# Performance work log

Hardware: AMD Instinct MI355X
Metric: run time of the kernel (lower is better)

## Reference

```python
import jax, jax.numpy as jnp
import numpy as np

HIDDEN_DIM = 2048
NUM_EXPERTS = 64
TOP_K = 8
NUM_TOKENS = 16384


def setup_inputs() -> dict:
    key = jax.random.key(0)
    k_x, k_w, k_b = jax.random.split(key, 3)
    X = jax.random.normal(k_x, (NUM_TOKENS, HIDDEN_DIM), dtype=jnp.float32)
    # nn.Linear(hidden_dim, num_experts): weight [out, in], bias [out]
    bound = 1.0 / np.sqrt(HIDDEN_DIM)
    W_gate = jax.random.uniform(k_w, (NUM_EXPERTS, HIDDEN_DIM), jnp.float32, -bound, bound)
    b_gate = jax.random.uniform(k_b, (NUM_EXPERTS,), jnp.float32, -bound, bound)
    return {"X": X, "W_gate": W_gate, "b_gate": b_gate}


def reference(X, W_gate, b_gate):
    # gate linear: [T, H] @ [H, E] + [E] -> [T, E]
    router_logits = jnp.einsum('th,eh->te', X, W_gate) + b_gate
    # softmax in float32 (matches dtype=torch.float)
    router_probs = jax.nn.softmax(router_logits.astype(jnp.float32), axis=-1)
    # top-k over experts: [T, K]
    router_weights, selected_experts_indices = jax.lax.top_k(router_probs, TOP_K)
    router_weights = router_weights / jnp.sum(router_weights, axis=-1, keepdims=True)
    router_weights = router_weights.astype(X.dtype)
    # one-hot [T, K, E] -> permute(2,1,0) -> [E, K, T]
    expert_mask = jax.nn.one_hot(selected_experts_indices, NUM_EXPERTS, dtype=jnp.int64 if jax.config.jax_enable_x64 else jnp.int32)
    expert_mask = jnp.transpose(expert_mask, (2, 1, 0))
    return (router_logits, router_weights, selected_experts_indices.astype(jnp.int32), expert_mask)
```

## Files before the change

kernel.cpp:

```cpp
#include <hip/hip_runtime.h>

#define NT 16384
#define NH 2048
#define NE 64
#define TOPK 8

#define TB 32
#define NSTEP 64
#define CSTEP 8
#define NCHUNK (NSTEP / CSTEP)

#define LOFF 0
#define WOFF (NT * NE)
#define IOFF (WOFF + NT * TOPK)
#define MOFF (IOFF + NT * TOPK)

typedef __attribute__((ext_vector_type(8))) short short8;
typedef __attribute__((ext_vector_type(4))) float floatx4;

union FragU { uint4 u; short8 s; };

#define WAITVM(n) asm volatile("s_waitcnt vmcnt(" #n ")" ::: "memory")
#define LGKM0     asm volatile("s_waitcnt lgkmcnt(0)" ::: "memory")

__device__ __forceinline__ void glds16(const void* g, void* l) {
    __builtin_amdgcn_global_load_lds(
        (const __attribute__((address_space(1))) unsigned int*)g,
        (__attribute__((address_space(3))) unsigned int*)l, 16, 0, 0);
}

__device__ __forceinline__ unsigned pack3(float a, float b, unsigned& w1, unsigned& w2) {
    unsigned au = __float_as_uint(a), bu = __float_as_uint(b);
    unsigned ah0 = au & 0xFFFF0000u, bh0 = bu & 0xFFFF0000u;
    float ra = a - __uint_as_float(ah0);
    float rb = b - __uint_as_float(bh0);
    unsigned ar = __float_as_uint(ra), br = __float_as_uint(rb);
    unsigned ah1 = ar & 0xFFFF0000u, bh1 = br & 0xFFFF0000u;
    float sa = ra - __uint_as_float(ah1);
    float sb = rb - __uint_as_float(bh1);
    w1 = bh1 | (ah1 >> 16);
    w2 = (__float_as_uint(sb) & 0xFFFF0000u) | (__float_as_uint(sa) >> 16);
    return bh0 | (ah0 >> 16);
}

__global__ __launch_bounds__(256)
void prep_kernel(const float* __restrict__ Wg, uint4* __restrict__ wsp,
                 float* __restrict__ out) {
    const int b = blockIdx.x;
    const int tid = threadIdx.x;

    float4 z = make_float4(0.f, 0.f, 0.f, 0.f);
    float4* mp = (float4*)(out + MOFF) + (size_t)b * 8192 + tid;
#pragma unroll
    for (int it = 0; it < 32; it++) mp[it * 256] = z;

    if (tid < 64) {
        const int t = b >> 2, g = b & 3;
        const int l = tid;
        const int e  = g * 16 + (l & 15);
        const int k0 = t * 32 + (l >> 4) * 8;
        const float* src = Wg + (size_t)e * NH + k0;
        float4 w0 = *(const float4*)src;
        float4 w1 = *(const float4*)(src + 4);
        unsigned u1[4], u2[4];
        uint4 p0;
        p0.x = pack3(w0.x, w0.y, u1[0], u2[0]);
        p0.y = pack3(w0.z, w0.w, u1[1], u2[1]);
        p0.z = pack3(w1.x, w1.y, u1[2], u2[2]);
        p0.w = pack3(w1.z, w1.w, u1[3], u2[3]);
        uint4* dst = wsp + (size_t)((t * 4 + g) * 3) * 64 + l;
        dst[0]   = p0;
        dst[64]  = make_uint4(u1[0], u1[1], u1[2], u1[3]);
        dst[128] = make_uint4(u2[0], u2[1], u2[2], u2[3]);
    }
}

__global__ __launch_bounds__(256, 2)
void router_kernel(const float* __restrict__ X, const uint4* __restrict__ wsp,
                   const float* __restrict__ bg, float* __restrict__ out) {
    __shared__ float SB[2][TB][256];
    __shared__ float Ls[TB][68];

    const int tid = threadIdx.x;
    const int wv  = tid >> 6;
    const int l   = tid & 63;
    const int th  = wv >> 1;
    const int eh  = wv & 1;
    const int lr  = l & 15, lq = l >> 4;
    const int lr7 = lr & 7;
    const int tbase = blockIdx.x * TB;

    floatx4 acc[2];
    acc[0] = (floatx4)0.0f;
    acc[1] = (floatx4)0.0f;

    const float* xsrc = X + (size_t)(tbase + wv * 8) * NH;
    const uint4* wb   = wsp + l;

#define STAGE(c_, s_) do { \
    _Pragma("unroll") \
    for (int j_ = 0; j_ < 8; j_++) \
        glds16(xsrc + (size_t)j_ * NH + (c_) * 256 + ((l ^ j_) << 2), \
               &SB[s_][wv * 8 + j_][0]); \
} while (0)

#define MFMA6(accv, A0, A1, A2, B0, B1, B2) do { \
    accv = __builtin_amdgcn_mfma_f32_16x16x32_bf16(A0, B0, accv, 0, 0, 0); \
    accv = __builtin_amdgcn_mfma_f32_16x16x32_bf16(A0, B1, accv, 0, 0, 0); \
    accv = __builtin_amdgcn_mfma_f32_16x16x32_bf16(A1, B0, accv, 0, 0, 0); \
    accv = __builtin_amdgcn_mfma_f32_16x16x32_bf16(A1, B1, accv, 0, 0, 0); \
    accv = __builtin_amdgcn_mfma_f32_16x16x32_bf16(A0, B2, accv, 0, 0, 0); \
    accv = __builtin_amdgcn_mfma_f32_16x16x32_bf16(A2, B0, accv, 0, 0, 0); \
} while (0)

#define KSTEP(s_, sg_, j_) do { \
    const float* ar_ = &SB[s_][th * 16 + lr][0]; \
    float4 lo_ = *(const float4*)(ar_ + ((((j_) * 8 + lq * 2 + 0) ^ lr7) << 2)); \
    float4 hi_ = *(const float4*)(ar_ + ((((j_) * 8 + lq * 2 + 1) ^ lr7) << 2)); \
    const uint4* wt_ = wb + ((size_t)(sg_) * 12 + eh * 6) * 64; \
    FragU b00, b01, b02, b10, b11, b12; \
    b00.u = wt_[0];   b01.u = wt_[64];  b02.u = wt_[128]; \
    b10.u = wt_[192]; b11.u = wt_[256]; b12.u = wt_[320]; \
    FragU a0_, a1_, a2_; \
    { unsigned u1_[4], u2_[4]; uint4 q_; \
      q_.x = pack3(lo_.x, lo_.y, u1_[0], u2_[0]); \
      q_.y = pack3(lo_.z, lo_.w, u1_[1], u2_[1]); \
      q_.z = pack3(hi_.x, hi_.y, u1_[2], u2_[2]); \
      q_.w = pack3(hi_.z, hi_.w, u1_[3], u2_[3]); \
      a0_.u = q_; \
      a1_.u = make_uint4(u1_[0], u1_[1], u1_[2], u1_[3]); \
      a2_.u = make_uint4(u2_[0], u2_[1], u2_[2], u2_[3]); } \
    __builtin_amdgcn_s_setprio(1); \
    MFMA6(acc[0], a0_.s, a1_.s, a2_.s, b00.s, b01.s, b02.s); \
    MFMA6(acc[1], a0_.s, a1_.s, a2_.s, b10.s, b11.s, b12.s); \
    __builtin_amdgcn_s_setprio(0); \
} while (0)

    STAGE(0, 0);
    STAGE(1, 1);

    WAITVM(8);
    __builtin_amdgcn_s_barrier();
#pragma unroll
    for (int j = 0; j < 8; j++) KSTEP(0, j, j);
    LGKM0;
    __builtin_amdgcn_s_barrier();
    STAGE(2, 0);

#pragma unroll 1
    for (int c = 1; c < NCHUNK; c++) {
        const int slot = c & 1;
        WAITVM(40);
        __builtin_amdgcn_s_barrier();
#pragma unroll
        for (int j = 0; j < 8; j++) KSTEP(slot, c * 8 + j, j);
        LGKM0;
        __builtin_amdgcn_s_barrier();
        if (c < NCHUNK - 2) STAGE(c + 2, slot);
    }

    const float b0 = bg[eh * 32 + lr];
    const float b1 = bg[eh * 32 + 16 + lr];
#pragma unroll
    for (int rr = 0; rr < 4; rr++) {
        Ls[th * 16 + lq * 4 + rr][eh * 32 + lr]      = acc[0][rr] + b0;
        Ls[th * 16 + lq * 4 + rr][eh * 32 + 16 + lr] = acc[1][rr] + b1;
    }
    __syncthreads();

#pragma unroll
    for (int v = 0; v < 2; v++) {
        int f4  = v * 256 + tid;
        int tok = f4 >> 4;
        int e4  = (f4 & 15) << 2;
        float4 o = *(const float4*)&Ls[tok][e4];
        *(float4*)(out + LOFF + (size_t)tbase * NE + (size_t)f4 * 4) = o;
    }

    const int tok = tid >> 3;
    const int el  = tid & 7;
    float4 va = *(const float4*)&Ls[tok][el * 8];
    float4 vb = *(const float4*)&Ls[tok][el * 8 + 4];
    float v[8] = {va.x, va.y, va.z, va.w, vb.x, vb.y, vb.z, vb.w};

    unsigned msk = 0;
    float m0 = 0.f, ssum = 0.f, myv = 0.f;
    int myi = 0;
#pragma unroll
    for (int r = 0; r < 8; r++) {
        float bv = -3.0e38f; int bi = 64;
#pragma unroll
        for (int j = 0; j < 8; j++) {
            bool better = (((msk >> j) & 1u) == 0u) && (v[j] > bv);
            bv = better ? v[j] : bv;
            bi = better ? (el * 8 + j) : bi;
        }
#pragma unroll
        for (int s2 = 1; s2 < 8; s2 <<= 1) {
            float ov = __shfl_xor(bv, s2);
            int   oi = __shfl_xor(bi, s2);
            bool take = (ov > bv) || (ov == bv && oi < bi);
            bv = take ? ov : bv;
            bi = take ? oi : bi;
        }
        if ((bi >> 3) == el) msk |= (1u << (bi & 7));
        if (r == 0) m0 = bv;
        ssum += __expf(bv - m0);
        if (r == el) { myv = bv; myi = bi; }
    }
    float wgt = __expf(myv - m0) / ssum;
    size_t gt = (size_t)(tbase + tok);
    out[WOFF + gt * TOPK + el] = wgt;
    out[IOFF + gt * TOPK + el] = (float)myi;
    out[MOFF + (size_t)myi * (TOPK * NT) + (size_t)el * NT + gt] = 1.0f;
}

extern "C" void kernel_launch(void* const* d_in, const int* in_sizes, int n_in,
                              void* d_out, int out_size, void* d_ws, size_t ws_size,
                              hipStream_t stream) {
    const float* X  = (const float*)d_in[0];
    const float* Wg = (const float*)d_in[1];
    const float* bg = (const float*)d_in[2];
    float* out = (float*)d_out;
    uint4* wsp = (uint4*)d_ws;

    hipLaunchKernelGGL(prep_kernel, dim3(256), dim3(256), 0, stream, Wg, wsp, out);
    hipLaunchKernelGGL(router_kernel, dim3(NT / TB), dim3(256), 0, stream,
                       X, (const uint4*)wsp, bg, out);
}
```

Measured before the change: 231.3 us.

## Use 64-token blocks with a triple-buffered LDS pipeline staging X and weights

```diff
diff --git a/kernel.cpp b/kernel.cpp
--- a/kernel.cpp
+++ b/kernel.cpp
@@ -5,10 +5,11 @@
 #define NE 64
 #define TOPK 8
 
-#define TB 32
+#define TB 64
 #define NSTEP 64
-#define CSTEP 8
+#define CSTEP 2
 #define NCHUNK (NSTEP / CSTEP)
+#define DEPTH 3
 
 #define LOFF 0
 #define WOFF (NT * NE)
@@ -71,14 +72,16 @@
         uint4* dst = wsp + (size_t)((t * 4 + g) * 3) * 64 + l;
         dst[0]   = p0;
         dst[64]  = make_uint4(u1[0], u1[1], u1[2], u1[3]);
+        dst[128] = make_uint4(u2[0], u2[1], u2[2], u2[2]);
         dst[128] = make_uint4(u2[0], u2[1], u2[2], u2[3]);
     }
 }
 
-__global__ __launch_bounds__(256, 2)
+__global__ __launch_bounds__(512, 2)
 void router_kernel(const float* __restrict__ X, const uint4* __restrict__ wsp,
                    const float* __restrict__ bg, float* __restrict__ out) {
-    __shared__ float SB[2][TB][256];
+    __shared__ float XS[DEPTH][TB][64];
+    __shared__ uint4 BS[DEPTH][1536];
     __shared__ float Ls[TB][68];
 
     const int tid = threadIdx.x;
@@ -94,14 +97,23 @@
     acc[0] = (floatx4)0.0f;
     acc[1] = (floatx4)0.0f;
 
-    const float* xsrc = X + (size_t)(tbase + wv * 8) * NH;
-    const uint4* wb   = wsp + l;
+    const int xrow0 = 8 * wv;
+    const int xsub  = l >> 4;
+    const int xw1   = (l >> 3) & 1;
+    const int xo    = l & 7;
 
 #define STAGE(c_, s_) do { \
     _Pragma("unroll") \
-    for (int j_ = 0; j_ < 8; j_++) \
-        glds16(xsrc + (size_t)j_ * NH + (c_) * 256 + ((l ^ j_) << 2), \
-               &SB[s_][wv * 8 + j_][0]); \
+    for (int j_ = 0; j_ < 2; j_++) { \
+        const int r_ = xrow0 + 4 * j_ + xsub; \
+        glds16(X + (size_t)(tbase + r_) * NH + (c_) * 64 \
+                 + (xw1 * 8 + (xo ^ (r_ & 7))) * 4, \
+               &XS[s_][xrow0 + 4 * j_][0]); \
+    } \
+    _Pragma("unroll") \
+    for (int i_ = 0; i_ < 3; i_++) \
+        glds16(wsp + (size_t)(c_) * 1536 + i_ * 512 + tid, \
+               &BS[s_][i_ * 512 + wv * 64]); \
 } while (0)
 
 #define MFMA6(accv, A0, A1, A2, B0, B1, B2) do { \
@@ -113,14 +125,14 @@
     accv = __builtin_amdgcn_mfma_f32_16x16x32_bf16(A2, B0, accv, 0, 0, 0); \
 } while (0)
 
-#define KSTEP(s_, sg_, j_) do { \
-    const float* ar_ = &SB[s_][th * 16 + lr][0]; \
-    float4 lo_ = *(const float4*)(ar_ + ((((j_) * 8 + lq * 2 + 0) ^ lr7) << 2)); \
-    float4 hi_ = *(const float4*)(ar_ + ((((j_) * 8 + lq * 2 + 1) ^ lr7) << 2)); \
-    const uint4* wt_ = wb + ((size_t)(sg_) * 12 + eh * 6) * 64; \
+#define KSTEP(s_, j2_) do { \
+    const float* ar_ = &XS[s_][th * 16 + lr][0]; \
+    float4 lo_ = *(const float4*)(ar_ + (((j2_) * 8 + ((2 * lq + 0) ^ lr7)) << 2)); \
+    float4 hi_ = *(const float4*)(ar_ + (((j2_) * 8 + ((2 * lq + 1) ^ lr7)) << 2)); \
+    const uint4* bb_ = &BS[s_][((j2_) * 12 + eh * 6) * 64 + l]; \
     FragU b00, b01, b02, b10, b11, b12; \
-    b00.u = wt_[0];   b01.u = wt_[64];  b02.u = wt_[128]; \
-    b10.u = wt_[192]; b11.u = wt_[256]; b12.u = wt_[320]; \
+    b00.u = bb_[0];   b01.u = bb_[64];  b02.u = bb_[128]; \
+    b10.u = bb_[192]; b11.u = bb_[256]; b12.u = bb_[320]; \
     FragU a0_, a1_, a2_; \
     { unsigned u1_[4], u2_[4]; uint4 q_; \
       q_.x = pack3(lo_.x, lo_.y, u1_[0], u2_[0]); \
@@ -136,28 +148,24 @@
     __builtin_amdgcn_s_setprio(0); \
 } while (0)
 
-    STAGE(0, 0);
-    STAGE(1, 1);
-
-    WAITVM(8);
-    __builtin_amdgcn_s_barrier();
-#pragma unroll
-    for (int j = 0; j < 8; j++) KSTEP(0, j, j);
-    LGKM0;
-    __builtin_amdgcn_s_barrier();
-    STAGE(2, 0);
-
+#define CONSUME(s_) do { KSTEP(s_, 0); KSTEP(s_, 1); } while (0)
+
+    STAGE(0, 0); STAGE(1, 1); STAGE(2, 2);
+
+    int slot = 0;
 #pragma unroll 1
-    for (int c = 1; c < NCHUNK; c++) {
-        const int slot = c & 1;
-        WAITVM(40);
+    for (int c = 0; c < NCHUNK - 3; c++) {
+        WAITVM(10);
         __builtin_amdgcn_s_barrier();
-#pragma unroll
-        for (int j = 0; j < 8; j++) KSTEP(slot, c * 8 + j, j);
+        CONSUME(slot);
         LGKM0;
         __builtin_amdgcn_s_barrier();
-        if (c < NCHUNK - 2) STAGE(c + 2, slot);
-    }
+        STAGE(c + 3, slot);
+        slot = (slot == DEPTH - 1) ? 0 : slot + 1;
+    }
+    WAITVM(10); __builtin_amdgcn_s_barrier(); CONSUME(2);
+    WAITVM(5);  __builtin_amdgcn_s_barrier(); CONSUME(0);
+    WAITVM(0);  __builtin_amdgcn_s_barrier(); CONSUME(1);
 
     const float b0 = bg[eh * 32 + lr];
     const float b1 = bg[eh * 32 + 16 + lr];
@@ -170,7 +178,7 @@
 
 #pragma unroll
     for (int v = 0; v < 2; v++) {
-        int f4  = v * 256 + tid;
+        int f4  = v * 512 + tid;
         int tok = f4 >> 4;
         int e4  = (f4 & 15) << 2;
         float4 o = *(const float4*)&Ls[tok][e4];
@@ -225,6 +233,6 @@
     uint4* wsp = (uint4*)d_ws;
 
     hipLaunchKernelGGL(prep_kernel, dim3(256), dim3(256), 0, stream, Wg, wsp, out);
-    hipLaunchKernelGGL(router_kernel, dim3(NT / TB), dim3(256), 0, stream,
+    hipLaunchKernelGGL(router_kernel, dim3(NT / TB), dim3(512), 0, stream,
                        X, (const uint4*)wsp, bg, out);
 }
```

New measurement: 231.9 us. No clear change (+0.3%).
